# Performance work log

Hardware: AMD Instinct MI355X
Metric: run time of the kernel (lower is better)

The kernel has to match this reference:

```python
import jax, jax.numpy as jnp
import numpy as np

D_MODEL = 2048
NHEAD = 32
GROUPS = 8
HEAD_DIM = D_MODEL // NHEAD  # 64
HPG = NHEAD // GROUPS        # heads per group = 4
ROPE_BASE = 10000.0


def _rope(x):
    # x: [B, H, S, D] -- rotate-half RoPE over full head dim, matching RoPE module
    S, D = x.shape[2], x.shape[3]
    theta = 1.0 / (ROPE_BASE ** (jnp.arange(0, D, 2, dtype=jnp.float32) / D))  # [D/2]
    idx_theta = jnp.arange(S, dtype=jnp.float32)[:, None] * theta[None, :]     # [S, D/2]
    ang = jnp.concatenate([idx_theta, idx_theta], axis=-1)                     # [S, D]
    cos = jnp.cos(ang)[None, None]  # [1,1,S,D]
    sin = jnp.sin(ang)[None, None]
    d2 = D // 2
    neg_half = jnp.concatenate([-x[..., d2:], x[..., :d2]], axis=-1)
    return x * cos + neg_half * sin


def setup_inputs() -> dict:
    key = jax.random.key(0)
    ks = jax.random.split(key, 9)
    B, S = 2, 2048
    s_in = 1.0 / np.sqrt(D_MODEL)
    return {
        "x": jax.random.normal(ks[0], (B, S, D_MODEL), jnp.float32),
        "Wq": jax.random.normal(ks[1], (D_MODEL, D_MODEL), jnp.float32) * s_in,
        "bq": jax.random.normal(ks[2], (D_MODEL,), jnp.float32) * 0.01,
        "Wk": jax.random.normal(ks[3], (HEAD_DIM * GROUPS, D_MODEL), jnp.float32) * s_in,
        "bk": jax.random.normal(ks[4], (HEAD_DIM * GROUPS,), jnp.float32) * 0.01,
        "Wv": jax.random.normal(ks[5], (HEAD_DIM * GROUPS, D_MODEL), jnp.float32) * s_in,
        "bv": jax.random.normal(ks[6], (HEAD_DIM * GROUPS,), jnp.float32) * 0.01,
        "Wo": jax.random.normal(ks[7], (D_MODEL, D_MODEL), jnp.float32) * s_in,
        "bo": jax.random.normal(ks[8], (D_MODEL,), jnp.float32) * 0.01,
    }


def reference(x, Wq, bq, Wk, bk, Wv, bv, Wo, bo):
    B, S, _ = x.shape
    # projections (torch Linear: x @ W.T + b)
    q = (x @ Wq.T + bq).reshape(B, S, NHEAD, HEAD_DIM).transpose(0, 2, 1, 3)   # [B,H,S,D]
    k = (x @ Wk.T + bk).reshape(B, S, GROUPS, HEAD_DIM).transpose(0, 2, 1, 3)  # [B,G,S,D]
    v = (x @ Wv.T + bv).reshape(B, S, GROUPS, HEAD_DIM).transpose(0, 2, 1, 3)  # [B,G,S,D]
    q = _rope(q)
    k = _rope(k)
    # grouped-query attention: share each k/v group across HPG query heads
    qg = q.reshape(B, GROUPS, HPG, S, HEAD_DIM)
    scale = 1.0 / np.sqrt(HEAD_DIM)
    scores = jnp.einsum('bghsd,bgtd->bghst', qg, k) * scale  # [B,G,Hpg,S,S]
    causal = jnp.tril(jnp.ones((S, S), dtype=bool))
    scores = jnp.where(causal, scores, jnp.finfo(scores.dtype).min)
    attn = jax.nn.softmax(scores, axis=-1)
    out = jnp.einsum('bghst,bgtd->bghsd', attn, v)           # [B,G,Hpg,S,D]
    out = out.reshape(B, NHEAD, S, HEAD_DIM).transpose(0, 2, 1, 3).reshape(B, S, D_MODEL)
    return out @ Wo.T + bo
```

## Files before the change

kernel.cpp:

```cpp
#include <hip/hip_runtime.h>

typedef unsigned short u16;
typedef __bf16 bf16x8 __attribute__((ext_vector_type(8)));
typedef float floatx4 __attribute__((ext_vector_type(4)));
typedef u16 u16x8 __attribute__((ext_vector_type(8)));
typedef u16 u16x4 __attribute__((ext_vector_type(4)));

#define D_MODEL 2048
#define S_LEN   2048
#define BATCH   2
#define NHEAD   32
#define GROUPS  8
#define HEAD_DIM 64
#define KV_DIM  512

__device__ __forceinline__ float bf2f(u16 h) {
  unsigned int u = ((unsigned int)h) << 16;
  return __builtin_bit_cast(float, u);
}
__device__ __forceinline__ u16 f2bf(float f) {
  unsigned int u = __builtin_bit_cast(unsigned int, f);
  u += 0x7fffu + ((u >> 16) & 1u);
  return (u16)(u >> 16);
}
__device__ __forceinline__ float fexp2(float x) {
  float r;
  asm("v_exp_f32 %0, %1" : "=v"(r) : "v"(x));
  return r;
}

#define GLD_LDS(gp, lp) \
  __builtin_amdgcn_global_load_lds((__attribute__((address_space(1))) void*)(gp), \
                                   (__attribute__((address_space(3))) void*)(lp), 16, 0, 0)

__global__ __launch_bounds__(256)
void cvt5_f32_bf16(const float* s0, const float* s1, const float* s2,
                   const float* s3, const float* s4,
                   u16* d0, u16* d1, u16* d2, u16* d3, u16* d4,
                   int n0, int n1, int n2, int n3, int n4,
                   float* ct, float* st)
{
  if (blockIdx.y == 5) {
    int idx = blockIdx.x * 256 + threadIdx.x;
    if (idx < S_LEN * 32) {
      int s = idx >> 5, d = idx & 31;
      float theta = __expf(-(float)d * 0.28782313662425574f);
      float sn, cs;
      sincosf((float)s * theta, &sn, &cs);
      ct[idx] = cs; st[idx] = sn;
    }
    return;
  }
  const float* s; u16* d; int n;
  switch (blockIdx.y) {
    case 0: s = s0; d = d0; n = n0; break;
    case 1: s = s1; d = d1; n = n1; break;
    case 2: s = s2; d = d2; n = n2; break;
    case 3: s = s3; d = d3; n = n3; break;
    default: s = s4; d = d4; n = n4; break;
  }
  long i = ((long)blockIdx.x * 256 + threadIdx.x) * 8;
  if (i >= n) return;
  floatx4 a = *(const floatx4*)(s + i);
  floatx4 b = *(const floatx4*)(s + i + 4);
  u16x8 r;
#pragma unroll
  for (int j = 0; j < 4; ++j) { r[j] = f2bf(a[j]); r[4 + j] = f2bf(b[j]); }
  *(u16x8*)(d + i) = r;
}

__global__ __launch_bounds__(256, 3)
void gemm_qkv(const u16* __restrict__ A, const u16* __restrict__ Wq,
              const u16* __restrict__ Wkv,
              const float* __restrict__ bq, const float* __restrict__ bk,
              const float* __restrict__ bv,
              u16* __restrict__ Qb, u16* __restrict__ Kb, u16* __restrict__ Vt,
              const float* __restrict__ ct, const float* __restrict__ st)
{
  const int K = D_MODEL;
  __shared__ __align__(16) u16 As[128 * 32];
  __shared__ __align__(16) u16 Bs[128 * 32];
  const int t = threadIdx.x;
  const int w = t >> 6, l = t & 63;
  const int lr = l & 15, lq = l >> 4;
  const int wm = (w >> 1) * 64, wn = (w & 1) * 64;
  const long bm = (long)blockIdx.x * 128;

  const bool isQ = blockIdx.y < 16;
  const long bn = isQ ? (long)blockIdx.y * 128 : (long)(blockIdx.y - 16) * 128;
  const u16* W = isQ ? Wq : Wkv;

  floatx4 acc[4][4] = {};

  const u16* a0 = A + (bm + (t >> 2)) * (long)K + (t & 3) * 8;
  const u16* a1 = a0 + 64L * K;
  const u16* pB0 = W + (bn + (t >> 2)) * (long)K + (t & 3) * 8;
  const u16* pB1 = pB0 + 64L * K;
  u16* As0 = As + w * 512;
  u16* As1 = As + 2048 + w * 512;
  u16* Bs0 = Bs + w * 512;
  u16* Bs1 = Bs + 2048 + w * 512;

  for (int k0 = 0; k0 < K; k0 += 32) {
    GLD_LDS(a0 + k0, As0);
    GLD_LDS(a1 + k0, As1);
    GLD_LDS(pB0 + k0, Bs0);
    GLD_LDS(pB1 + k0, Bs1);
    __syncthreads();

    bf16x8 av[4], bv8[4];
#pragma unroll
    for (int i = 0; i < 4; ++i)
      av[i] = *(const bf16x8*)(As + (wm + i * 16 + lr) * 32 + lq * 8);
#pragma unroll
    for (int j = 0; j < 4; ++j)
      bv8[j] = *(const bf16x8*)(Bs + (wn + j * 16 + lr) * 32 + lq * 8);
#pragma unroll
    for (int i = 0; i < 4; ++i)
#pragma unroll
      for (int j = 0; j < 4; ++j)
        acc[i][j] = __builtin_amdgcn_mfma_f32_16x16x32_bf16(av[i], bv8[j], acc[i][j], 0, 0, 0);
    __syncthreads();
  }

  if (isQ || bn < KV_DIM) {
    const float* bias = isQ ? bq : bk;
    u16* dst = isQ ? Qb : Kb;
    const long ldc = isQ ? D_MODEL : KV_DIM;
    float bb[4];
#pragma unroll
    for (int j = 0; j < 4; ++j)
      bb[j] = bias[bn + wn + j * 16 + lr];
#pragma unroll
    for (int i = 0; i < 4; ++i) {
#pragma unroll
      for (int rr = 0; rr < 4; ++rr) {
        long row = bm + wm + i * 16 + lq * 4 + rr;
        int srow = (int)row & (S_LEN - 1);
        float c0 = ct[srow * 32 + lr],      sn0 = st[srow * 32 + lr];
        float c1 = ct[srow * 32 + 16 + lr], sn1 = st[srow * 32 + 16 + lr];
        float v0 = acc[i][0][rr] + bb[0];
        float v1 = acc[i][1][rr] + bb[1];
        float v2 = acc[i][2][rr] + bb[2];
        float v3 = acc[i][3][rr] + bb[3];
        u16* cp = dst + row * ldc + bn + wn + lr;
        cp[0]  = f2bf(v0 * c0 - v2 * sn0);
        cp[16] = f2bf(v1 * c1 - v3 * sn1);
        cp[32] = f2bf(v2 * c0 + v0 * sn0);
        cp[48] = f2bf(v3 * c1 + v1 * sn1);
      }
    }
  } else {
    float bb[4];
#pragma unroll
    for (int j = 0; j < 4; ++j)
      bb[j] = bv[bn - KV_DIM + wn + j * 16 + lr];
#pragma unroll
    for (int i = 0; i < 4; ++i) {
      int row0 = (int)bm + wm + i * 16 + lq * 4;
      int b = row0 >> 11, s0r = row0 & (S_LEN - 1);
#pragma unroll
      for (int j = 0; j < 4; ++j) {
        int vcol = (int)bn - KV_DIM + wn + j * 16 + lr;
        u16x4 pv;
#pragma unroll
        for (int rr = 0; rr < 4; ++rr)
          pv[rr] = f2bf(acc[i][j][rr] + bb[j]);
        *(u16x4*)(Vt + ((long)b * KV_DIM + vcol) * S_LEN + s0r) = pv;
      }
    }
  }
}

__global__ __launch_bounds__(256, 3)
void gemm_out(const u16* __restrict__ A, const u16* __restrict__ W,
              const float* __restrict__ bias, float* __restrict__ C,
              int K, int ldc)
{
  __shared__ __align__(16) u16 As[128 * 32];
  __shared__ __align__(16) u16 Bs[128 * 32];
  const int t = threadIdx.x;
  const int w = t >> 6, l = t & 63;
  const int lr = l & 15, lq = l >> 4;
  const int wm = (w >> 1) * 64, wn = (w & 1) * 64;
  const long bm = (long)blockIdx.x * 128;
  const long bn = (long)blockIdx.y * 128;

  floatx4 acc[4][4] = {};

  const u16* a0 = A + (bm + (t >> 2)) * (long)K + (t & 3) * 8;
  const u16* a1 = a0 + 64L * K;
  const u16* pB0 = W + (bn + (t >> 2)) * (long)K + (t & 3) * 8;
  const u16* pB1 = pB0 + 64L * K;
  u16* As0 = As + w * 512;
  u16* As1 = As + 2048 + w * 512;
  u16* Bs0 = Bs + w * 512;
  u16* Bs1 = Bs + 2048 + w * 512;

  for (int k0 = 0; k0 < K; k0 += 32) {
    GLD_LDS(a0 + k0, As0);
    GLD_LDS(a1 + k0, As1);
    GLD_LDS(pB0 + k0, Bs0);
    GLD_LDS(pB1 + k0, Bs1);
    __syncthreads();

    bf16x8 av[4], bv[4];
#pragma unroll
    for (int i = 0; i < 4; ++i)
      av[i] = *(const bf16x8*)(As + (wm + i * 16 + lr) * 32 + lq * 8);
#pragma unroll
    for (int j = 0; j < 4; ++j)
      bv[j] = *(const bf16x8*)(Bs + (wn + j * 16 + lr) * 32 + lq * 8);
#pragma unroll
    for (int i = 0; i < 4; ++i)
#pragma unroll
      for (int j = 0; j < 4; ++j)
        acc[i][j] = __builtin_amdgcn_mfma_f32_16x16x32_bf16(av[i], bv[j], acc[i][j], 0, 0, 0);
    __syncthreads();
  }

  float bb[4];
#pragma unroll
  for (int j = 0; j < 4; ++j)
    bb[j] = bias[bn + wn + j * 16 + lr];
#pragma unroll
  for (int i = 0; i < 4; ++i) {
#pragma unroll
    for (int rr = 0; rr < 4; ++rr) {
      long row = bm + wm + i * 16 + lq * 4 + rr;
      long cidx = row * (long)ldc + bn + wn + lr;
      float* cp = C + cidx;
#pragma unroll
      for (int j = 0; j < 4; ++j)
        cp[j * 16] = acc[i][j][rr] + bb[j];
    }
  }
}

__global__ __launch_bounds__(256, 3)
void gqa_attn(const u16* Q, const u16* __restrict__ Kc,
              const u16* __restrict__ Vt, u16* O)
{
  __shared__ __align__(16) u16 KV[2][16 * 512];
  __shared__ __align__(16) u16 Ps[4][2][16 * 72];

  const int pr = blockIdx.x;
  const int bh = blockIdx.y;
  const int b = bh >> 5, h = bh & 31, g = h >> 2;

  const int t = threadIdx.x;
  const int w = t >> 6, l = t & 63;
  const int lr = l & 15, lq = l >> 4;

  const u16* Kp = Kc + ((long)b * S_LEN) * KV_DIM + g * HEAD_DIM;
  const u16* Vp = Vt + ((long)b * KV_DIM + g * HEAD_DIM) * S_LEN;

  long sb[4];
  {
    const int sig2 = ((l >> 2) ^ (l >> 4)) & 1;
    const int sig1 = ((l >> 1) ^ (l >> 3)) & 1;
    const int sig0 = (l ^ sig2) & 1;
    const int row = ((l >> 2) & 14) | sig2;
    const int cl = ((sig1 << 1) | sig0) * 8;
#pragma unroll
    for (int q = 0; q < 4; ++q) {
      const int r = (w & 1) * 4 + q;
      const int jj = r >> 1, cc = r & 1;
      sb[q] = (w < 2) ? ((long)(jj * 16 + row) * KV_DIM + cc * 32 + cl)
                      : ((long)(jj * 16 + row) * S_LEN + cc * 32 + cl);
    }
  }
  const u16* sp = (w < 2) ? Kp : Vp;
  const long smul = (w < 2) ? (long)64 * KV_DIM : 64;
  const int dbase = ((w < 2) ? 0 : 4096) + (w & 1) * 2048;
  const int koff = ((4 * lr + lq) ^ (lr & 7)) * 8;

#define STAGE(bufi, kt_) do { \
    const long soff_ = (long)(kt_) * smul; \
    GLD_LDS(sp + soff_ + sb[0], &KV[bufi][dbase + 0 * 512]); \
    GLD_LDS(sp + soff_ + sb[1], &KV[bufi][dbase + 1 * 512]); \
    GLD_LDS(sp + soff_ + sb[2], &KV[bufi][dbase + 2 * 512]); \
    GLD_LDS(sp + soff_ + sb[3], &KV[bufi][dbase + 3 * 512]); \
  } while (0)

#define TILE(ktv, D0, D1) do { \
    const u16* buf_ = &KV[(ktv) & 1][0]; \
    floatx4 z0[4] = {}, z1[4] = {}; \
    _Pragma("unroll") \
    for (int j = 0; j < 4; ++j) { \
      bf16x8 kf0 = *(const bf16x8*)(buf_ + j * 1024 + koff); \
      bf16x8 kf1 = *(const bf16x8*)(buf_ + j * 1024 + 512 + koff); \
      if (!(D1) && (!(D0) || j <= w)) { \
        z0[j] = __builtin_amdgcn_mfma_f32_16x16x32_bf16(kf0, qf00, z0[j], 0, 0, 0); \
        z0[j] = __builtin_amdgcn_mfma_f32_16x16x32_bf16(kf1, qf01, z0[j], 0, 0, 0); \
      } \
      if (!(D1) || j <= w) { \
        z1[j] = __builtin_amdgcn_mfma_f32_16x16x32_bf16(kf0, qf10, z1[j], 0, 0, 0); \
        z1[j] = __builtin_amdgcn_mfma_f32_16x16x32_bf16(kf1, qf11, z1[j], 0, 0, 0); \
      } \
    } \
    if (!(D1)) { \
      _Pragma("unroll") \
      for (int j = 0; j < 4; ++j) { \
        u16x4 pk; \
        _Pragma("unroll") \
        for (int rr = 0; rr < 4; ++rr) { \
          float ps; \
          if ((D0) && (j * 16 + lq * 4 + rr > w * 16 + lr)) ps = 0.f; \
          else ps = fexp2(z0[j][rr] * 0.18033688011112042f - 23.083120654223414f); \
          ls0 += ps; \
          pk[rr] = __builtin_bit_cast(u16, (__bf16)ps); \
        } \
        *(u16x4*)&Ps[w][0][lr * 72 + j * 16 + lq * 4] = pk; \
      } \
    } \
    _Pragma("unroll") \
    for (int j = 0; j < 4; ++j) { \
      u16x4 pk; \
      _Pragma("unroll") \
      for (int rr = 0; rr < 4; ++rr) { \
        float ps; \
        if ((D1) && (j * 16 + lq * 4 + rr > w * 16 + lr)) ps = 0.f; \
        else ps = fexp2(z1[j][rr] * 0.18033688011112042f - 23.083120654223414f); \
        ls1 += ps; \
        pk[rr] = __builtin_bit_cast(u16, (__bf16)ps); \
      } \
      *(u16x4*)&Ps[w][1][lr * 72 + j * 16 + lq * 4] = pk; \
    } \
    bf16x8 pa00 = *(const bf16x8*)&Ps[w][0][lr * 72 + lq * 8]; \
    bf16x8 pa01 = *(const bf16x8*)&Ps[w][0][lr * 72 + 32 + lq * 8]; \
    bf16x8 pa10 = *(const bf16x8*)&Ps[w][1][lr * 72 + lq * 8]; \
    bf16x8 pa11 = *(const bf16x8*)&Ps[w][1][lr * 72 + 32 + lq * 8]; \
    const u16* vbuf_ = buf_ + 4096; \
    _Pragma("unroll") \
    for (int j = 0; j < 4; ++j) { \
      bf16x8 vb0 = *(const bf16x8*)(vbuf_ + j * 1024 + koff); \
      bf16x8 vb1 = *(const bf16x8*)(vbuf_ + j * 1024 + 512 + koff); \
      if (!(D1)) { \
        o0[j] = __builtin_amdgcn_mfma_f32_16x16x32_bf16(pa00, vb0, o0[j], 0, 0, 0); \
        if (!(D0) || w >= 2) \
          o0[j] = __builtin_amdgcn_mfma_f32_16x16x32_bf16(pa01, vb1, o0[j], 0, 0, 0); \
      } \
      o1[j] = __builtin_amdgcn_mfma_f32_16x16x32_bf16(pa10, vb0, o1[j], 0, 0, 0); \
      if (!(D1) || w >= 2) \
        o1[j] = __builtin_amdgcn_mfma_f32_16x16x32_bf16(pa11, vb1, o1[j], 0, 0, 0); \
    } \
  } while (0)

#pragma unroll 1
  for (int seg = 0; seg < 2; ++seg) {
    const int qt = seg ? (15 - pr) : pr;
    const u16* Qp = Q + ((long)b * S_LEN + qt * 128) * D_MODEL + h * HEAD_DIM;
    u16* Op = O + ((long)b * S_LEN + qt * 128) * D_MODEL + h * HEAD_DIM;

    bf16x8 qf00, qf01, qf10, qf11;
    {
      const u16* qr0 = Qp + (long)(w * 16 + lr) * D_MODEL;
      qf00 = *(const bf16x8*)(qr0 + lq * 8);
      qf01 = *(const bf16x8*)(qr0 + 32 + lq * 8);
      const u16* qr1 = qr0 + (long)64 * D_MODEL;
      qf10 = *(const bf16x8*)(qr1 + lq * 8);
      qf11 = *(const bf16x8*)(qr1 + 32 + lq * 8);
    }

    floatx4 o0[4] = {}, o1[4] = {};
    float ls0 = 0.f, ls1 = 0.f;
    const int NKT = 2 * qt + 2;

    if (seg) __syncthreads();
    STAGE(0, 0);
    for (int kt = 0; kt < NKT - 2; ++kt) {
      __syncthreads();
      STAGE((kt + 1) & 1, kt + 1);
      TILE(kt, false, false);
    }
    __syncthreads();
    STAGE((NKT - 1) & 1, NKT - 1);
    TILE(NKT - 2, true, false);
    __syncthreads();
    TILE(NKT - 1, false, true);

#pragma unroll
    for (int s = 0; s < 2; ++s) {
      float ls = s ? ls1 : ls0;
      ls += __shfl_xor(ls, 16);
      ls += __shfl_xor(ls, 32);
      const floatx4* oo = s ? o1 : o0;
#pragma unroll
      for (int rr = 0; rr < 4; ++rr) {
        float lrow = __shfl(ls, lq * 4 + rr);
        float inv = 1.f / lrow;
        long row = s * 64 + w * 16 + lq * 4 + rr;
        u16* op = Op + row * (long)D_MODEL + lr;
#pragma unroll
        for (int j = 0; j < 4; ++j)
          op[j * 16] = f2bf(oo[j][rr] * inv);
      }
    }
  }
#undef TILE
#undef STAGE
}

extern "C" void kernel_launch(void* const* d_in, const int* in_sizes, int n_in,
                              void* d_out, int out_size, void* d_ws, size_t ws_size,
                              hipStream_t stream)
{
  const float* x  = (const float*)d_in[0];
  const float* Wq = (const float*)d_in[1];
  const float* bq = (const float*)d_in[2];
  const float* Wk = (const float*)d_in[3];
  const float* bk = (const float*)d_in[4];
  const float* Wv = (const float*)d_in[5];
  const float* bv = (const float*)d_in[6];
  const float* Wo = (const float*)d_in[7];
  const float* bo = (const float*)d_in[8];
  float* out = (float*)d_out;

  const int Sx  = BATCH * S_LEN * D_MODEL;
  const int SWq = D_MODEL * D_MODEL;
  const int SWk = KV_DIM * D_MODEL;
  const int SWv = KV_DIM * D_MODEL;
  const int SWo = D_MODEL * D_MODEL;

  u16* xb  = (u16*)d_ws;
  u16* Wqb = xb  + Sx;
  u16* Wkb = Wqb + SWq;
  u16* Wvb = Wkb + SWk;
  u16* Wob = Wvb + SWv;
  u16* Qb  = Wob + SWo;
  u16* Kb  = Qb + (size_t)4096 * 2048;
  u16* Vtb = Kb + (size_t)4096 * 512;
  float* ctab = (float*)(Vtb + (size_t)BATCH * KV_DIM * S_LEN);
  float* stab = ctab + S_LEN * 32;
  u16* AO  = Qb;

  const int M = BATCH * S_LEN;
  dim3 blk(256);
  cvt5_f32_bf16<<<dim3(4096, 6), blk, 0, stream>>>(x, Wq, Wk, Wv, Wo,
                                                   xb, Wqb, Wkb, Wvb, Wob,
                                                   Sx, SWq, SWk, SWv, SWo,
                                                   ctab, stab);
  gemm_qkv<<<dim3(M / 128, 24), blk, 0, stream>>>(xb, Wqb, Wkb, bq, bk, bv,
                                                  Qb, Kb, Vtb, ctab, stab);
  gqa_attn<<<dim3(8, BATCH * NHEAD), blk, 0, stream>>>(Qb, Kb, Vtb, AO);
  gemm_out<<<dim3(M / 128, D_MODEL / 128), blk, 0, stream>>>(AO, Wob, bo, out, D_MODEL, D_MODEL);
}
```

Baseline: 281.0 us.

## Double GEMM K-step per barrier and compute softmax row sums via MFMA

Both projection GEMMs now load two 32-wide K slices into twice the LDS per iteration, which halves the number of __syncthreads barriers across the K loop. In the attention kernel the per-element scalar row-sum accumulation and the final cross-lane shuffles are replaced by extra MFMAs that multiply the bf16 P tile with a ones vector. That moves the sum work onto the matrix cores and also makes the denominator use the same bf16-rounded P values as the PV product. The cost is double the LDS per block, which may reduce occupancy at launch bounds of 3, plus a few extra MFMAs per tile.

```diff
diff --git a/kernel.cpp b/kernel.cpp
--- a/kernel.cpp
+++ b/kernel.cpp
@@ -78,8 +78,8 @@
               const float* __restrict__ ct, const float* __restrict__ st)
 {
   const int K = D_MODEL;
-  __shared__ __align__(16) u16 As[128 * 32];
-  __shared__ __align__(16) u16 Bs[128 * 32];
+  __shared__ __align__(16) u16 As[2 * 128 * 32];
+  __shared__ __align__(16) u16 Bs[2 * 128 * 32];
   const int t = threadIdx.x;
   const int w = t >> 6, l = t & 63;
   const int lr = l & 15, lq = l >> 4;
@@ -101,25 +101,34 @@
   u16* Bs0 = Bs + w * 512;
   u16* Bs1 = Bs + 2048 + w * 512;
 
-  for (int k0 = 0; k0 < K; k0 += 32) {
+  for (int k0 = 0; k0 < K; k0 += 64) {
     GLD_LDS(a0 + k0, As0);
     GLD_LDS(a1 + k0, As1);
     GLD_LDS(pB0 + k0, Bs0);
     GLD_LDS(pB1 + k0, Bs1);
-    __syncthreads();
-
-    bf16x8 av[4], bv8[4];
-#pragma unroll
-    for (int i = 0; i < 4; ++i)
-      av[i] = *(const bf16x8*)(As + (wm + i * 16 + lr) * 32 + lq * 8);
-#pragma unroll
-    for (int j = 0; j < 4; ++j)
-      bv8[j] = *(const bf16x8*)(Bs + (wn + j * 16 + lr) * 32 + lq * 8);
-#pragma unroll
-    for (int i = 0; i < 4; ++i)
+    GLD_LDS(a0 + k0 + 32, As0 + 4096);
+    GLD_LDS(a1 + k0 + 32, As1 + 4096);
+    GLD_LDS(pB0 + k0 + 32, Bs0 + 4096);
+    GLD_LDS(pB1 + k0 + 32, Bs1 + 4096);
+    __syncthreads();
+
+#pragma unroll
+    for (int kk = 0; kk < 2; ++kk) {
+      const u16* as = As + kk * 4096;
+      const u16* bs = Bs + kk * 4096;
+      bf16x8 av[4], bv8[4];
+#pragma unroll
+      for (int i = 0; i < 4; ++i)
+        av[i] = *(const bf16x8*)(as + (wm + i * 16 + lr) * 32 + lq * 8);
 #pragma unroll
       for (int j = 0; j < 4; ++j)
-        acc[i][j] = __builtin_amdgcn_mfma_f32_16x16x32_bf16(av[i], bv8[j], acc[i][j], 0, 0, 0);
+        bv8[j] = *(const bf16x8*)(bs + (wn + j * 16 + lr) * 32 + lq * 8);
+#pragma unroll
+      for (int i = 0; i < 4; ++i)
+#pragma unroll
+        for (int j = 0; j < 4; ++j)
+          acc[i][j] = __builtin_amdgcn_mfma_f32_16x16x32_bf16(av[i], bv8[j], acc[i][j], 0, 0, 0);
+    }
     __syncthreads();
   }
 
@@ -177,8 +186,8 @@
               const float* __restrict__ bias, float* __restrict__ C,
               int K, int ldc)
 {
-  __shared__ __align__(16) u16 As[128 * 32];
-  __shared__ __align__(16) u16 Bs[128 * 32];
+  __shared__ __align__(16) u16 As[2 * 128 * 32];
+  __shared__ __align__(16) u16 Bs[2 * 128 * 32];
   const int t = threadIdx.x;
   const int w = t >> 6, l = t & 63;
   const int lr = l & 15, lq = l >> 4;
@@ -197,25 +206,34 @@
   u16* Bs0 = Bs + w * 512;
   u16* Bs1 = Bs + 2048 + w * 512;
 
-  for (int k0 = 0; k0 < K; k0 += 32) {
+  for (int k0 = 0; k0 < K; k0 += 64) {
     GLD_LDS(a0 + k0, As0);
     GLD_LDS(a1 + k0, As1);
     GLD_LDS(pB0 + k0, Bs0);
     GLD_LDS(pB1 + k0, Bs1);
-    __syncthreads();
-
-    bf16x8 av[4], bv[4];
-#pragma unroll
-    for (int i = 0; i < 4; ++i)
-      av[i] = *(const bf16x8*)(As + (wm + i * 16 + lr) * 32 + lq * 8);
-#pragma unroll
-    for (int j = 0; j < 4; ++j)
-      bv[j] = *(const bf16x8*)(Bs + (wn + j * 16 + lr) * 32 + lq * 8);
-#pragma unroll
-    for (int i = 0; i < 4; ++i)
+    GLD_LDS(a0 + k0 + 32, As0 + 4096);
+    GLD_LDS(a1 + k0 + 32, As1 + 4096);
+    GLD_LDS(pB0 + k0 + 32, Bs0 + 4096);
+    GLD_LDS(pB1 + k0 + 32, Bs1 + 4096);
+    __syncthreads();
+
+#pragma unroll
+    for (int kk = 0; kk < 2; ++kk) {
+      const u16* as = As + kk * 4096;
+      const u16* bs = Bs + kk * 4096;
+      bf16x8 av[4], bv[4];
+#pragma unroll
+      for (int i = 0; i < 4; ++i)
+        av[i] = *(const bf16x8*)(as + (wm + i * 16 + lr) * 32 + lq * 8);
 #pragma unroll
       for (int j = 0; j < 4; ++j)
-        acc[i][j] = __builtin_amdgcn_mfma_f32_16x16x32_bf16(av[i], bv[j], acc[i][j], 0, 0, 0);
+        bv[j] = *(const bf16x8*)(bs + (wn + j * 16 + lr) * 32 + lq * 8);
+#pragma unroll
+      for (int i = 0; i < 4; ++i)
+#pragma unroll
+        for (int j = 0; j < 4; ++j)
+          acc[i][j] = __builtin_amdgcn_mfma_f32_16x16x32_bf16(av[i], bv[j], acc[i][j], 0, 0, 0);
+    }
     __syncthreads();
   }
 
@@ -274,6 +292,10 @@
   const long smul = (w < 2) ? (long)64 * KV_DIM : 64;
   const int dbase = ((w < 2) ? 0 : 4096) + (w & 1) * 2048;
   const int koff = ((4 * lr + lq) ^ (lr & 7)) * 8;
+
+  bf16x8 onesf;
+#pragma unroll
+  for (int e = 0; e < 8; ++e) onesf[e] = (__bf16)1.0f;
 
 #define STAGE(bufi, kt_) do { \
     const long soff_ = (long)(kt_) * smul; \
@@ -308,7 +330,6 @@
           float ps; \
           if ((D0) && (j * 16 + lq * 4 + rr > w * 16 + lr)) ps = 0.f; \
           else ps = fexp2(z0[j][rr] * 0.18033688011112042f - 23.083120654223414f); \
-          ls0 += ps; \
           pk[rr] = __builtin_bit_cast(u16, (__bf16)ps); \
         } \
         *(u16x4*)&Ps[w][0][lr * 72 + j * 16 + lq * 4] = pk; \
@@ -322,7 +343,6 @@
         float ps; \
         if ((D1) && (j * 16 + lq * 4 + rr > w * 16 + lr)) ps = 0.f; \
         else ps = fexp2(z1[j][rr] * 0.18033688011112042f - 23.083120654223414f); \
-        ls1 += ps; \
         pk[rr] = __builtin_bit_cast(u16, (__bf16)ps); \
       } \
       *(u16x4*)&Ps[w][1][lr * 72 + j * 16 + lq * 4] = pk; \
@@ -331,6 +351,14 @@
     bf16x8 pa01 = *(const bf16x8*)&Ps[w][0][lr * 72 + 32 + lq * 8]; \
     bf16x8 pa10 = *(const bf16x8*)&Ps[w][1][lr * 72 + lq * 8]; \
     bf16x8 pa11 = *(const bf16x8*)&Ps[w][1][lr * 72 + 32 + lq * 8]; \
+    if (!(D1)) { \
+      lsa0 = __builtin_amdgcn_mfma_f32_16x16x32_bf16(pa00, onesf, lsa0, 0, 0, 0); \
+      if (!(D0) || w >= 2) \
+        lsa0 = __builtin_amdgcn_mfma_f32_16x16x32_bf16(pa01, onesf, lsa0, 0, 0, 0); \
+    } \
+    lsa1 = __builtin_amdgcn_mfma_f32_16x16x32_bf16(pa10, onesf, lsa1, 0, 0, 0); \
+    if (!(D1) || w >= 2) \
+      lsa1 = __builtin_amdgcn_mfma_f32_16x16x32_bf16(pa11, onesf, lsa1, 0, 0, 0); \
     const u16* vbuf_ = buf_ + 4096; \
     _Pragma("unroll") \
     for (int j = 0; j < 4; ++j) { \
@@ -364,7 +392,7 @@
     }
 
     floatx4 o0[4] = {}, o1[4] = {};
-    float ls0 = 0.f, ls1 = 0.f;
+    floatx4 lsa0 = {}, lsa1 = {};
     const int NKT = 2 * qt + 2;
 
     if (seg) __syncthreads();
@@ -382,14 +410,11 @@
 
 #pragma unroll
     for (int s = 0; s < 2; ++s) {
-      float ls = s ? ls1 : ls0;
-      ls += __shfl_xor(ls, 16);
-      ls += __shfl_xor(ls, 32);
+      const floatx4 lsv = s ? lsa1 : lsa0;
       const floatx4* oo = s ? o1 : o0;
 #pragma unroll
       for (int rr = 0; rr < 4; ++rr) {
-        float lrow = __shfl(ls, lq * 4 + rr);
-        float inv = 1.f / lrow;
+        float inv = 1.f / lsv[rr];
         long row = s * 64 + w * 16 + lq * 4 + rr;
         u16* op = Op + row * (long)D_MODEL + lr;
 #pragma unroll
```

New measurement: 280.1 us. About the same (-0.3%).
